# Performance work log

Hardware: AMD Instinct MI355X
Metric: run time of the kernel (lower is better)

Reference implementation:

```python
import jax, jax.numpy as jnp
import numpy as np

N_NODES = 100000
H = 256
E = 500000

def setup_inputs() -> dict:
    key = jax.random.key(0)
    ks = jax.random.split(key, 7)
    z_src = jax.random.normal(ks[0], (N_NODES, H), dtype=jnp.float32)
    z_dst = jax.random.normal(ks[1], (N_NODES, H), dtype=jnp.float32)
    edge_label_index = jax.random.randint(ks[2], (2, E), 0, N_NODES, dtype=jnp.int64)
    # Linear params, scaled like torch default init (~1/sqrt(fan_in))
    w1 = jax.random.normal(ks[3], (H, 2 * H), dtype=jnp.float32) * (1.0 / np.sqrt(2 * H))
    b1 = jax.random.normal(ks[4], (H,), dtype=jnp.float32) * (1.0 / np.sqrt(2 * H))
    w2 = jax.random.normal(ks[5], (1, H), dtype=jnp.float32) * (1.0 / np.sqrt(H))
    b2 = jax.random.normal(ks[6], (1,), dtype=jnp.float32) * (1.0 / np.sqrt(H))
    return {"z_src": z_src, "z_dst": z_dst, "edge_label_index": edge_label_index,
            "w1": w1, "b1": b1, "w2": w2, "b2": b2}

def reference(z_src, z_dst, edge_label_index, w1, b1, w2, b2):
    row, col = edge_label_index[0], edge_label_index[1]
    # gather edge endpoint features and concat -> [E, 2H]
    z = jnp.concatenate([z_src[row], z_dst[col]], axis=-1)
    z = jax.nn.relu(jnp.einsum('eh,oh->eo', z, w1) + b1)  # [E, H]
    z = jnp.einsum('eh,oh->eo', z, w2) + b2               # [E, 1]
    return jax.nn.sigmoid(z).reshape(-1)
```

## Files before the change

### kernel.cpp

```cpp
#include <hip/hip_runtime.h>

#define E_TOT 500000
#define N_NODES 100000
#define NUNITS_H 3125

typedef __attribute__((ext_vector_type(16))) float f32x16;
typedef __attribute__((ext_vector_type(8))) short short8;
typedef __attribute__((ext_vector_type(4))) float f32x4;

__device__ __forceinline__ unsigned short f2bf(float f) {
  union { float f; unsigned u; } x; x.f = f;
  unsigned r = x.u + 0x7fffu + ((x.u >> 16) & 1u);
  return (unsigned short)(r >> 16);
}

__device__ __forceinline__ float bf2f(unsigned short s) {
  union { unsigned u; float f; } x; x.u = ((unsigned)s) << 16;
  return x.f;
}

__device__ __forceinline__ void gl_lds16(const void* g, void* l) {
  __builtin_amdgcn_global_load_lds(
      (const __attribute__((address_space(1))) void*)g,
      (__attribute__((address_space(3))) void*)l, 16, 0, 0);
}

__global__ void k_repack_w1h(const float* __restrict__ w1,
                             unsigned short* __restrict__ w1r2) {
  int o = blockIdx.x * 256 + threadIdx.x;
  int half = o >> 16;
  int kb = (o >> 11) & 31;
  int n = (o >> 3) & 255;
  int j = o & 7;
  w1r2[o] = f2bf(w1[n * 512 + half * 256 + kb * 8 + j]);
}

__global__ __launch_bounds__(512, 1) void k_node_gemm(
    const float* __restrict__ zsrc, const float* __restrict__ zdst,
    const unsigned short* __restrict__ w1r2, const float* __restrict__ b1,
    unsigned short* __restrict__ Uo, unsigned short* __restrict__ Vo) {
  __shared__ __align__(16) unsigned short Bp[65536];
  __shared__ __align__(16) unsigned short Ap[8192];
  __shared__ __align__(16) unsigned short Ct[8192];

  const int half = blockIdx.x >> 7;
  const int bh = blockIdx.x & 127;
  const float* Z = half ? zdst : zsrc;
  unsigned short* O = half ? Vo : Uo;

  const unsigned tid = threadIdx.x;
  const unsigned l = tid & 63u;
  const unsigned wv = tid >> 6;
  const unsigned l31 = l & 31u;
  const unsigned hi = l >> 5;
  const unsigned arow = tid & 31u;
  const unsigned ak2 = tid >> 5;

  {
    const unsigned short* src = w1r2 + (unsigned)half * 65536u;
#pragma unroll
    for (int q = 0; q < 16; ++q) {
      unsigned off = ((unsigned)q * 512u + tid) * 8u;
      gl_lds16(src + off, Bp + off);
    }
  }

  const float bi = half ? 0.f : b1[wv * 32u + l31];

  f32x4 ap[4];
#define LOAD_A(uu)                                                        \
  {                                                                       \
    const f32x4* p_ =                                                     \
        (const f32x4*)(Z + ((long)(uu)*32 + arow) * 256 + ak2 * 16u);     \
    ap[0] = p_[0]; ap[1] = p_[1]; ap[2] = p_[2]; ap[3] = p_[3];           \
  }
#define WRITE_A()                                                         \
  {                                                                       \
    _Pragma("unroll") for (int g = 0; g < 2; ++g) {                       \
      short8 sa;                                                          \
      sa[0] = (short)f2bf(ap[2*g].x);   sa[1] = (short)f2bf(ap[2*g].y);   \
      sa[2] = (short)f2bf(ap[2*g].z);   sa[3] = (short)f2bf(ap[2*g].w);   \
      sa[4] = (short)f2bf(ap[2*g+1].x); sa[5] = (short)f2bf(ap[2*g+1].y); \
      sa[6] = (short)f2bf(ap[2*g+1].z); sa[7] = (short)f2bf(ap[2*g+1].w); \
      *(short8*)&Ap[((2u*ak2 + (unsigned)g)*32u + arow)*8u] = sa;         \
    }                                                                     \
  }

  int u = bh;
  LOAD_A(u);
  WRITE_A();
  __syncthreads();

  for (; u < NUNITS_H; u += 128) {
    int un = u + 128;
    if (un >= NUNITS_H) un = u;
    LOAD_A(un);
    __builtin_amdgcn_sched_barrier(0);

    f32x16 acc = {0.f, 0.f, 0.f, 0.f, 0.f, 0.f, 0.f, 0.f,
                  0.f, 0.f, 0.f, 0.f, 0.f, 0.f, 0.f, 0.f};
#pragma unroll
    for (int kk = 0; kk < 16; ++kk) {
      unsigned ks = 2u * (unsigned)kk + hi;
      short8 af = *(const short8*)&Ap[(ks * 32u + l31) * 8u];
      short8 bf = *(const short8*)&Bp[(ks * 256u + wv * 32u + l31) * 8u];
      acc = __builtin_amdgcn_mfma_f32_32x32x16_bf16(af, bf, acc, 0, 0, 0);
    }
    __syncthreads();

    WRITE_A();
#pragma unroll
    for (int r = 0; r < 16; ++r) {
      unsigned row32 = (unsigned)((r & 3) + 8 * (r >> 2)) + 4u * hi;
      Ct[row32 * 256u + wv * 32u + l31] = f2bf(acc[r] + bi);
    }
    __syncthreads();

    {
      const long gbase = (long)u * 32 * 256;
#pragma unroll
      for (int p = 0; p < 2; ++p) {
        unsigned s = (unsigned)p * 512u + tid;
        unsigned row = s >> 5;
        unsigned seg = s & 31u;
        short8 vv = *(const short8*)&Ct[row * 256u + seg * 8u];
        *(short8*)(O + gbase + row * 256u + seg * 8u) = vv;
      }
    }
  }
#undef LOAD_A
#undef WRITE_A
}

#define EK_ITER 16
__global__ __launch_bounds__(256, 6) void k_edge(
    const unsigned short* __restrict__ U, const unsigned short* __restrict__ V,
    const int* __restrict__ eli, const float* __restrict__ w2,
    const float* __restrict__ b2, float* __restrict__ out) {
  const int tid = threadIdx.x;
  const int g = tid >> 4;
  const int j = tid & 15;
  float w2v[16];
#pragma unroll
  for (int q = 0; q < 8; ++q) {
    w2v[q] = w2[8 * j + q];
    w2v[8 + q] = w2[128 + 8 * j + q];
  }
  const float b2v = b2[0];
  const long base = (long)blockIdx.x * (16 * EK_ITER) + g;

#define CLAMP_E(k) \
  (((base + 16 * (k)) < E_TOT) ? (base + 16 * (k)) : (long)(E_TOT - 1))

  long eP = CLAMP_E(0);
  int rA = eli[eP], cA = eli[E_TOT + eP];
  long eQ = CLAMP_E(1);
  int rB = eli[eQ], cB = eli[E_TOT + eQ];
  short8 uA0 = *(const short8*)(U + (long)rA * 256 + 8 * j);
  short8 uA1 = *(const short8*)(U + (long)rA * 256 + 128 + 8 * j);
  short8 vA0 = *(const short8*)(V + (long)cA * 256 + 8 * j);
  short8 vA1 = *(const short8*)(V + (long)cA * 256 + 128 + 8 * j);
  short8 uB0, uB1, vB0, vB1;

#pragma unroll
  for (int it2 = 0; it2 < EK_ITER / 2; ++it2) {
    {
      long eN = CLAMP_E(2 * it2 + 2);
      int rN = eli[eN], cN = eli[E_TOT + eN];
      uB0 = *(const short8*)(U + (long)rB * 256 + 8 * j);
      uB1 = *(const short8*)(U + (long)rB * 256 + 128 + 8 * j);
      vB0 = *(const short8*)(V + (long)cB * 256 + 8 * j);
      vB1 = *(const short8*)(V + (long)cB * 256 + 128 + 8 * j);
      rB = rN; cB = cN;
      float p = 0.f;
#pragma unroll
      for (int q = 0; q < 8; ++q) {
        float a0 = bf2f((unsigned short)uA0[q]) + bf2f((unsigned short)vA0[q]);
        float a1 = bf2f((unsigned short)uA1[q]) + bf2f((unsigned short)vA1[q]);
        p = fmaf(fmaxf(a0, 0.f), w2v[q], p);
        p = fmaf(fmaxf(a1, 0.f), w2v[8 + q], p);
      }
      p += __shfl_xor(p, 1);
      p += __shfl_xor(p, 2);
      p += __shfl_xor(p, 4);
      p += __shfl_xor(p, 8);
      long e = base + 16 * (2 * it2);
      if (j == 0 && e < E_TOT) out[e] = 1.f / (1.f + __expf(-(p + b2v)));
    }
    {
      long eN = CLAMP_E(2 * it2 + 3);
      int rN = eli[eN], cN = eli[E_TOT + eN];
      uA0 = *(const short8*)(U + (long)rB * 256 + 8 * j);
      uA1 = *(const short8*)(U + (long)rB * 256 + 128 + 8 * j);
      vA0 = *(const short8*)(V + (long)cB * 256 + 8 * j);
      vA1 = *(const short8*)(V + (long)cB * 256 + 128 + 8 * j);
      rB = rN; cB = cN;
      float p = 0.f;
#pragma unroll
      for (int q = 0; q < 8; ++q) {
        float a0 = bf2f((unsigned short)uB0[q]) + bf2f((unsigned short)vB0[q]);
        float a1 = bf2f((unsigned short)uB1[q]) + bf2f((unsigned short)vB1[q]);
        p = fmaf(fmaxf(a0, 0.f), w2v[q], p);
        p = fmaf(fmaxf(a1, 0.f), w2v[8 + q], p);
      }
      p += __shfl_xor(p, 1);
      p += __shfl_xor(p, 2);
      p += __shfl_xor(p, 4);
      p += __shfl_xor(p, 8);
      long e = base + 16 * (2 * it2 + 1);
      if (j == 0 && e < E_TOT) out[e] = 1.f / (1.f + __expf(-(p + b2v)));
    }
  }
#undef CLAMP_E
}

extern "C" void kernel_launch(void* const* d_in, const int* in_sizes, int n_in,
                              void* d_out, int out_size, void* d_ws,
                              size_t ws_size, hipStream_t stream) {
  const float* zsrc = (const float*)d_in[0];
  const float* zdst = (const float*)d_in[1];
  const int* eli = (const int*)d_in[2];
  const float* w1 = (const float*)d_in[3];
  const float* b1 = (const float*)d_in[4];
  const float* w2 = (const float*)d_in[5];
  const float* b2 = (const float*)d_in[6];
  float* out = (float*)d_out;

  const size_t uv_bytes = (size_t)N_NODES * 256 * 2;
  unsigned short* U = (unsigned short*)d_ws;
  unsigned short* V = (unsigned short*)((char*)d_ws + uv_bytes);
  unsigned short* w1r2 = (unsigned short*)((char*)d_ws + 2 * uv_bytes);

  k_repack_w1h<<<512, 256, 0, stream>>>(w1, w1r2);
  k_node_gemm<<<256, 512, 0, stream>>>(zsrc, zdst, w1r2, b1, U, V);
  int nbe = (E_TOT + 16 * EK_ITER - 1) / (16 * EK_ITER);
  k_edge<<<nbe, 256, 0, stream>>>(U, V, eli, w2, b2, out);
}
```

Before: 155.2 us.

## Keep W1 fragments in registers and double-buffer A/C tiles in node GEMM

The node GEMM now loads each wave's W1 B-fragments once into registers instead of staging the full 128KB weight half in LDS. Freeing that LDS allows two blocks per CU, and the A and C tiles are double-buffered so one of the two barriers per iteration can be dropped. This costs 64 extra VGPRs per thread for the B fragments, which under launch_bounds(512,2) could cause spills. The grid is still only 256 blocks, so the higher occupancy may not be fully used.

```diff
diff --git a/kernel.cpp b/kernel.cpp
--- a/kernel.cpp
+++ b/kernel.cpp
@@ -17,12 +17,6 @@
 __device__ __forceinline__ float bf2f(unsigned short s) {
   union { unsigned u; float f; } x; x.u = ((unsigned)s) << 16;
   return x.f;
-}
-
-__device__ __forceinline__ void gl_lds16(const void* g, void* l) {
-  __builtin_amdgcn_global_load_lds(
-      (const __attribute__((address_space(1))) void*)g,
-      (__attribute__((address_space(3))) void*)l, 16, 0, 0);
 }
 
 __global__ void k_repack_w1h(const float* __restrict__ w1,
@@ -35,13 +29,12 @@
   w1r2[o] = f2bf(w1[n * 512 + half * 256 + kb * 8 + j]);
 }
 
-__global__ __launch_bounds__(512, 1) void k_node_gemm(
+__global__ __launch_bounds__(512, 2) void k_node_gemm(
     const float* __restrict__ zsrc, const float* __restrict__ zdst,
     const unsigned short* __restrict__ w1r2, const float* __restrict__ b1,
     unsigned short* __restrict__ Uo, unsigned short* __restrict__ Vo) {
-  __shared__ __align__(16) unsigned short Bp[65536];
-  __shared__ __align__(16) unsigned short Ap[8192];
-  __shared__ __align__(16) unsigned short Ct[8192];
+  __shared__ __align__(16) unsigned short Ap[2][8192];
+  __shared__ __align__(16) unsigned short Ct[2][8192];
 
   const int half = blockIdx.x >> 7;
   const int bh = blockIdx.x & 127;
@@ -56,12 +49,14 @@
   const unsigned arow = tid & 31u;
   const unsigned ak2 = tid >> 5;
 
+  short8 brg[16];
   {
-    const unsigned short* src = w1r2 + (unsigned)half * 65536u;
-#pragma unroll
-    for (int q = 0; q < 16; ++q) {
-      unsigned off = ((unsigned)q * 512u + tid) * 8u;
-      gl_lds16(src + off, Bp + off);
+    const unsigned short* bb = w1r2 + (unsigned)half * 65536u;
+#pragma unroll
+    for (int k = 0; k < 16; ++k) {
+      unsigned ks = (unsigned)k * 2u + hi;
+      brg[k] = *(const short8*)(bb + (ks * 256u + wv * 32u + l31) * 8u);
+      asm volatile("" : "+v"(brg[k]));
     }
   }
 
@@ -74,7 +69,7 @@
         (const f32x4*)(Z + ((long)(uu)*32 + arow) * 256 + ak2 * 16u);     \
     ap[0] = p_[0]; ap[1] = p_[1]; ap[2] = p_[2]; ap[3] = p_[3];           \
   }
-#define WRITE_A()                                                         \
+#define WRITE_A(bf_)                                                      \
   {                                                                       \
     _Pragma("unroll") for (int g = 0; g < 2; ++g) {                       \
       short8 sa;                                                          \
@@ -82,13 +77,14 @@
       sa[2] = (short)f2bf(ap[2*g].z);   sa[3] = (short)f2bf(ap[2*g].w);   \
       sa[4] = (short)f2bf(ap[2*g+1].x); sa[5] = (short)f2bf(ap[2*g+1].y); \
       sa[6] = (short)f2bf(ap[2*g+1].z); sa[7] = (short)f2bf(ap[2*g+1].w); \
-      *(short8*)&Ap[((2u*ak2 + (unsigned)g)*32u + arow)*8u] = sa;         \
+      *(short8*)&Ap[bf_][((2u*ak2 + (unsigned)g)*32u + arow)*8u] = sa;    \
     }                                                                     \
   }
 
   int u = bh;
+  int cur = 0;
   LOAD_A(u);
-  WRITE_A();
+  WRITE_A(0);
   __syncthreads();
 
   for (; u < NUNITS_H; u += 128) {
@@ -102,18 +98,16 @@
 #pragma unroll
     for (int kk = 0; kk < 16; ++kk) {
       unsigned ks = 2u * (unsigned)kk + hi;
-      short8 af = *(const short8*)&Ap[(ks * 32u + l31) * 8u];
-      short8 bf = *(const short8*)&Bp[(ks * 256u + wv * 32u + l31) * 8u];
-      acc = __builtin_amdgcn_mfma_f32_32x32x16_bf16(af, bf, acc, 0, 0, 0);
-    }
-    __syncthreads();
-
-    WRITE_A();
+      short8 af = *(const short8*)&Ap[cur][(ks * 32u + l31) * 8u];
+      acc = __builtin_amdgcn_mfma_f32_32x32x16_bf16(af, brg[kk], acc, 0, 0, 0);
+    }
+
 #pragma unroll
     for (int r = 0; r < 16; ++r) {
       unsigned row32 = (unsigned)((r & 3) + 8 * (r >> 2)) + 4u * hi;
-      Ct[row32 * 256u + wv * 32u + l31] = f2bf(acc[r] + bi);
-    }
+      Ct[cur][row32 * 256u + wv * 32u + l31] = f2bf(acc[r] + bi);
+    }
+    WRITE_A(cur ^ 1);
     __syncthreads();
 
     {
@@ -123,10 +117,11 @@
         unsigned s = (unsigned)p * 512u + tid;
         unsigned row = s >> 5;
         unsigned seg = s & 31u;
-        short8 vv = *(const short8*)&Ct[row * 256u + seg * 8u];
+        short8 vv = *(const short8*)&Ct[cur][row * 256u + seg * 8u];
         *(short8*)(O + gbase + row * 256u + seg * 8u) = vv;
       }
     }
+    cur ^= 1;
   }
 #undef LOAD_A
 #undef WRITE_A
```

Measured after the change: 149.1 us, median of 2. -3.9%, faster.
